# Kernel tuning notes

Measured on AMD Instinct MI355X. Metric: run time of the kernel, lower is better.

The kernel has to match this reference:

```python
import jax, jax.numpy as jnp
import numpy as np

NUM_HEADS = 8


def setup_inputs() -> dict:
    key = jax.random.key(0)
    k1, k2, k3 = jax.random.split(key, 3)
    B, C, H, W = 2, 256, 64, 64
    x = jax.random.normal(k1, (B, C, H, W), dtype=jnp.float32)
    # 1x1 conv kernels flattened to [out_ch, in_ch]
    w_qkv = jax.random.normal(k2, (3 * C, C), dtype=jnp.float32) * (1.0 / np.sqrt(C))
    w_proj = jax.random.normal(k3, (C, C), dtype=jnp.float32) * (1.0 / np.sqrt(C))
    return {"x": x, "w_qkv": w_qkv, "w_proj": w_proj}


def reference(x, w_qkv, w_proj):
    B, C, H, W = x.shape
    h = NUM_HEADS
    hc = C // h  # head_channels
    scale = hc ** (-0.5)

    # 1x1 conv == per-pixel matmul over channels
    qkv = jnp.einsum('bchw,oc->bohw', x, w_qkv)  # [B, 3C, H, W]
    q, k, v = jnp.split(qkv, 3, axis=1)          # each [B, C, H, W]

    def to_heads(t):
        # 'b (h c) x y -> b h (x y) c'
        return t.reshape(B, h, hc, H * W).transpose(0, 1, 3, 2)

    q, k, v = to_heads(q), to_heads(k), to_heads(v)  # [B, h, N, hc]

    attn = jax.nn.softmax(jnp.einsum('bhnc,bhmc->bhnm', q, k) * scale, axis=-1)
    out = jnp.einsum('bhnm,bhmc->bhnc', attn, v)     # [B, h, N, hc]

    # 'b h (x y) c -> b (h c) x y'
    out = out.transpose(0, 1, 3, 2).reshape(B, C, H, W)
    return jnp.einsum('bchw,oc->bohw', out, w_proj)
```

## Files before the change

### kernel.cpp

```cpp
#include <hip/hip_runtime.h>
#include <hip/hip_bf16.h>


typedef short s8v __attribute__((ext_vector_type(8)));
typedef float f32x16 __attribute__((ext_vector_type(16)));
typedef float f32x2 __attribute__((ext_vector_type(2)));
typedef unsigned int u32;
typedef unsigned int u32x4 __attribute__((ext_vector_type(4)));

__device__ __forceinline__ u32 cvt_pk_bf16(float lo, float hi){
  u32 d;
  asm("v_cvt_pk_bf16_f32 %0, %1, %2" : "=v"(d) : "v"(lo), "v"(hi));
  return d;
}

__device__ __forceinline__ int frag_off(int row, int c){
  return ((c>>4)<<9) + (((c>>3)&1)<<8) + (row<<3) + (c&7);
}

__global__ __launch_bounds__(256) void k_transpose_cast(const float* __restrict__ x,
                                                        __hip_bfloat16* __restrict__ xt){
  __shared__ float tile[64][65];
  const int b = blockIdx.z;
  const int c0 = blockIdx.y * 64, p0 = blockIdx.x * 64;
  const int tx = threadIdx.x & 63, ty = threadIdx.x >> 6;
  const float* src = x + ((size_t)b*256 + c0)*4096 + p0;
#pragma unroll
  for(int i=0;i<16;i++){
    int r = i*4 + ty;
    tile[r][tx] = src[(size_t)r*4096 + tx];
  }
  __syncthreads();
  __hip_bfloat16* dstb = xt + (size_t)b*1048576;
#pragma unroll
  for(int it=0; it<2; ++it){
    int id = it*256 + threadIdx.x;
    int pl = id & 63, cc = id >> 6;
    int c = c0 + cc*8;
    u32x4 wv;
    wv.x = cvt_pk_bf16(tile[cc*8+0][pl], tile[cc*8+1][pl]);
    wv.y = cvt_pk_bf16(tile[cc*8+2][pl], tile[cc*8+3][pl]);
    wv.z = cvt_pk_bf16(tile[cc*8+4][pl], tile[cc*8+5][pl]);
    wv.w = cvt_pk_bf16(tile[cc*8+6][pl], tile[cc*8+7][pl]);
    int panel = (p0 + pl) >> 5;
    *(u32x4*)(dstb + (size_t)panel*8192 + frag_off(pl & 31, c)) = wv;
  }
}

__global__ __launch_bounds__(256) void k_cast_w(const float* __restrict__ wqkv,
                                                const float* __restrict__ wproj,
                                                __hip_bfloat16* __restrict__ wq,
                                                __hip_bfloat16* __restrict__ wp){
  int e = blockIdx.x*256 + threadIdx.x;
  const float* srcw; __hip_bfloat16* dstw;
  if(e < 24576){ srcw = wqkv; dstw = wq; }
  else { e -= 24576; srcw = wproj; dstw = wp; }
  int o = e >> 5, c0 = (e & 31)*8;
  const float* s = srcw + (size_t)o*256 + c0;
  u32x4 wv;
  wv.x = cvt_pk_bf16(s[0], s[1]);
  wv.y = cvt_pk_bf16(s[2], s[3]);
  wv.z = cvt_pk_bf16(s[4], s[5]);
  wv.w = cvt_pk_bf16(s[6], s[7]);
  *(u32x4*)(dstw + (size_t)(o>>5)*8192 + frag_off(o & 31, c0)) = wv;
}

__global__ __launch_bounds__(256) void k_qkv(const __hip_bfloat16* __restrict__ w,
                                             const __hip_bfloat16* __restrict__ xt,
                                             __hip_bfloat16* __restrict__ qb,
                                             __hip_bfloat16* __restrict__ kb,
                                             __hip_bfloat16* __restrict__ vt){
  const int wave = threadIdx.x >> 6, lane = threadIdx.x & 63;
  const int l31 = lane & 31, hi = lane >> 5;
  const int t = blockIdx.x*4 + wave;
  const int ntp = t & 127, mtp = t >> 7;
  const __hip_bfloat16* a0 = w  + (size_t)(2*mtp)*8192 + lane*8;
  const __hip_bfloat16* b0 = xt + (size_t)(2*ntp)*8192 + lane*8;
  f32x16 acc00, acc01, acc10, acc11;
#pragma unroll
  for(int i=0;i<16;i++){ acc00[i]=0.f; acc01[i]=0.f; acc10[i]=0.f; acc11[i]=0.f; }
#pragma unroll
  for(int kk=0;kk<16;kk++){
    s8v af0 = *(const s8v*)(a0 + kk*512);
    s8v af1 = *(const s8v*)(a0 + 8192 + kk*512);
    s8v bf0 = *(const s8v*)(b0 + kk*512);
    s8v bf1 = *(const s8v*)(b0 + 8192 + kk*512);
    acc00 = __builtin_amdgcn_mfma_f32_32x32x16_bf16(af0, bf0, acc00, 0,0,0);
    acc01 = __builtin_amdgcn_mfma_f32_32x32x16_bf16(af0, bf1, acc01, 0,0,0);
    acc10 = __builtin_amdgcn_mfma_f32_32x32x16_bf16(af1, bf0, acc10, 0,0,0);
    acc11 = __builtin_amdgcn_mfma_f32_32x32x16_bf16(af1, bf1, acc11, 0,0,0);
  }
  const int region = mtp >> 2;
  const float s = (region==0) ? (0.17677669529663687f * 1.4426950408889634f) : 1.0f;
#pragma unroll
  for(int mi=0; mi<2; ++mi){
#pragma unroll
    for(int ni=0; ni<2; ++ni){
      const f32x16& acc = (mi==0) ? (ni==0?acc00:acc01) : (ni==0?acc10:acc11);
      const int mt = 2*mtp + mi, nt = 2*ntp + ni;
      const int bb = nt >> 7, ktile = nt & 127, h = mt & 7;
      const size_t tbase = (size_t)(bb*8 + h)*131072 + (size_t)ktile*1024;
      if(region < 2){
        __hip_bfloat16* dst = (region==0 ? qb : kb) + tbase + l31*8 + 4*hi;
#pragma unroll
        for(int g=0; g<4; ++g){
          uint2 wv;
          wv.x = cvt_pk_bf16(acc[4*g+0]*s, acc[4*g+1]*s);
          wv.y = cvt_pk_bf16(acc[4*g+2]*s, acc[4*g+3]*s);
          *(uint2*)(dst + (g>>1)*512 + (g&1)*256) = wv;
        }
      } else {
        const int j = l31 >> 4, hv = (l31 >> 2) & 1, tt = ((l31>>3)&1)*4 + (l31&3);
        __hip_bfloat16* dst = vt + tbase + j*512 + hv*256 + tt;
#pragma unroll
        for(int r=0;r<16;++r){
          int c = (r&3) + 8*(r>>2) + 4*hi;
          dst[c*8] = __float2bfloat16(acc[r]);
        }
      }
    }
  }
}

__global__ __launch_bounds__(256) void k_attn(const __hip_bfloat16* __restrict__ qb,
                                              const __hip_bfloat16* __restrict__ kb,
                                              const __hip_bfloat16* __restrict__ vt,
                                              __hip_bfloat16* __restrict__ ost){
  __shared__ float part[4][32][33];
  __shared__ float lsl[4][32];
  const int wave = threadIdx.x >> 6, lane = threadIdx.x & 63;
  const int l31 = lane & 31, hi = lane >> 5;
  const int bh = blockIdx.x >> 7, qc = blockIdx.x & 127;

  const __hip_bfloat16* qt = qb + (size_t)bh*131072 + (size_t)qc*1024 + (size_t)lane*8;
  const s8v qf0 = *(const s8v*)qt;
  const s8v qf1 = *(const s8v*)(qt + 512);

  const __hip_bfloat16* kbase = kb + (size_t)bh*131072 + (size_t)lane*8;
  const __hip_bfloat16* vbase = vt + (size_t)bh*131072 + (size_t)lane*8;

  f32x16 zf;
#pragma unroll
  for(int i=0;i<16;i++) zf[i]=0.f;
  f32x16 oacc;
#pragma unroll
  for(int i=0;i<16;i++) oacc[i]=0.f;
  f32x2 s0 = {0.f,0.f}, s1 = {0.f,0.f}, s2 = {0.f,0.f}, s3 = {0.f,0.f};

  const int kt0 = wave*32;
#pragma unroll 2
  for(int i=0;i<32;++i){
    const int kt = kt0 + i;
    const __hip_bfloat16* kp = kbase + (size_t)kt*1024;
    s8v kf0 = *(const s8v*)kp, kf1 = *(const s8v*)(kp + 512);
    f32x16 sa = __builtin_amdgcn_mfma_f32_32x32x16_bf16(kf0, qf0, zf, 0,0,0);
    sa = __builtin_amdgcn_mfma_f32_32x32x16_bf16(kf1, qf1, sa, 0,0,0);

    float pv[16];
#pragma unroll
    for(int r=0;r<16;++r) pv[r] = __builtin_amdgcn_exp2f(sa[r]);
    s0 += (f32x2){pv[0],pv[1]};  s1 += (f32x2){pv[2],pv[3]};
    s2 += (f32x2){pv[4],pv[5]};  s3 += (f32x2){pv[6],pv[7]};
    s0 += (f32x2){pv[8],pv[9]};  s1 += (f32x2){pv[10],pv[11]};
    s2 += (f32x2){pv[12],pv[13]}; s3 += (f32x2){pv[14],pv[15]};

    u32x4 w0, w1;
    w0.x = cvt_pk_bf16(pv[0],  pv[1]);   w0.y = cvt_pk_bf16(pv[2],  pv[3]);
    w0.z = cvt_pk_bf16(pv[4],  pv[5]);   w0.w = cvt_pk_bf16(pv[6],  pv[7]);
    w1.x = cvt_pk_bf16(pv[8],  pv[9]);   w1.y = cvt_pk_bf16(pv[10], pv[11]);
    w1.z = cvt_pk_bf16(pv[12], pv[13]);  w1.w = cvt_pk_bf16(pv[14], pv[15]);
    s8v pa0 = __builtin_bit_cast(s8v, w0);
    s8v pa1 = __builtin_bit_cast(s8v, w1);

    const __hip_bfloat16* vp = vbase + (size_t)kt*1024;
    s8v vf0 = *(const s8v*)vp, vf1 = *(const s8v*)(vp + 512);
    oacc = __builtin_amdgcn_mfma_f32_32x32x16_bf16(vf0, pa0, oacc, 0,0,0);
    oacc = __builtin_amdgcn_mfma_f32_32x32x16_bf16(vf1, pa1, oacc, 0,0,0);
  }

  float lsum = (s0.x + s0.y) + (s1.x + s1.y) + (s2.x + s2.y) + (s3.x + s3.y);
  lsum += __shfl_xor(lsum, 32, 64);
  lsl[wave][l31] = lsum;
#pragma unroll
  for(int r=0;r<16;++r){
    int c = (r&3) + 8*(r>>2) + 4*hi;
    part[wave][l31][c] = oacc[r];
  }
  __syncthreads();

  const int b = bh >> 3, h = bh & 7;
  __hip_bfloat16* obase = ost + (size_t)(b*128 + qc)*8192;
#pragma unroll
  for(int it=0; it<4; ++it){
    int e = it*256 + threadIdx.x;
    int q = e >> 5, c = e & 31;
    float o = (part[0][q][c] + part[1][q][c]) + (part[2][q][c] + part[3][q][c]);
    float L = (lsl[0][q] + lsl[1][q]) + (lsl[2][q] + lsl[3][q]);
    obase[(h*2 + (c>>4))*512 + ((c>>3)&1)*256 + q*8 + (c&7)] = __float2bfloat16(o / L);
  }
}

__global__ __launch_bounds__(256) void k_proj(const __hip_bfloat16* __restrict__ w,
                                              const __hip_bfloat16* __restrict__ ost,
                                              float* __restrict__ out){
  const int wave = threadIdx.x >> 6, lane = threadIdx.x & 63;
  const int l31 = lane & 31, hi = lane >> 5;
  const int t = blockIdx.x*4 + wave;
  const int nt = t & 255, mt = t >> 8;
  const __hip_bfloat16* arow = w   + (size_t)mt*8192 + lane*8;
  const __hip_bfloat16* brow = ost + (size_t)nt*8192 + lane*8;
  f32x16 acc;
#pragma unroll
  for(int i=0;i<16;i++) acc[i]=0.f;
#pragma unroll
  for(int kk=0;kk<16;kk++){
    s8v a = *(const s8v*)(arow + kk*512);
    s8v b = *(const s8v*)(brow + kk*512);
    acc = __builtin_amdgcn_mfma_f32_32x32x16_bf16(a, b, acc, 0,0,0);
  }
  const int pg = nt*32 + l31;
  const int bb = pg >> 12, p = pg & 4095;
  float* dst = out + (size_t)bb*1048576 + p;
#pragma unroll
  for(int r=0;r<16;++r){
    int o = mt*32 + (r&3) + 8*(r>>2) + 4*hi;
    dst[(size_t)o*4096] = acc[r];
  }
}

extern "C" void kernel_launch(void* const* d_in, const int* in_sizes, int n_in,
                              void* d_out, int out_size, void* d_ws, size_t ws_size,
                              hipStream_t stream){
  const float* x     = (const float*)d_in[0];
  const float* wqkv  = (const float*)d_in[1];
  const float* wproj = (const float*)d_in[2];
  float* out = (float*)d_out;

  const size_t SZ_XT = (size_t)8192*256*2;
  const size_t SZ_VT = (size_t)16*32*4096*2;
  const size_t SZ_WQ = (size_t)768*256*2;
  const size_t SZ_WP = (size_t)256*256*2;
  if(ws_size < SZ_XT + SZ_VT + SZ_WQ + SZ_WP) return;

  char* ws = (char*)d_ws;
  __hip_bfloat16* xt  = (__hip_bfloat16*)ws;
  __hip_bfloat16* vt  = (__hip_bfloat16*)(ws + SZ_XT);
  __hip_bfloat16* wqb = (__hip_bfloat16*)(ws + SZ_XT + SZ_VT);
  __hip_bfloat16* wpb = (__hip_bfloat16*)(ws + SZ_XT + SZ_VT + SZ_WQ);
  __hip_bfloat16* qb  = (__hip_bfloat16*)d_out;
  __hip_bfloat16* kb  = qb + (size_t)2*1024*1024;
  __hip_bfloat16* ost = xt;

  k_cast_w<<<128, 256, 0, stream>>>(wqkv, wproj, wqb, wpb);
  k_transpose_cast<<<dim3(64,4,2), 256, 0, stream>>>(x, xt);
  k_qkv<<<384, 256, 0, stream>>>(wqb, xt, qb, kb, vt);
  k_attn<<<2048, 256, 0, stream>>>(qb, kb, vt, ost);
  k_proj<<<512, 256, 0, stream>>>(wpb, ost, out);
}
```

Measured before the change: 85.28 us.

## Process two query tiles per attention block to reuse K/V fragments

Each attention block now handles 64 queries (two 32-query tiles) instead of 32. Each loaded K and V fragment feeds two sets of MFMAs, which halves K/V global traffic per query and halves the grid. Block indices are also remapped so that consecutive blocks spread across batch-heads, which may help L2/XCD locality. The cost is doubled accumulator and score register pressure, with launch bounds set to 4 blocks per CU, and fewer blocks in flight.

```diff
diff --git a/kernel.cpp b/kernel.cpp
--- a/kernel.cpp
+++ b/kernel.cpp
@@ -122,19 +122,22 @@
   }
 }
 
-__global__ __launch_bounds__(256) void k_attn(const __hip_bfloat16* __restrict__ qb,
-                                              const __hip_bfloat16* __restrict__ kb,
-                                              const __hip_bfloat16* __restrict__ vt,
-                                              __hip_bfloat16* __restrict__ ost){
-  __shared__ float part[4][32][33];
-  __shared__ float lsl[4][32];
+__global__ __launch_bounds__(256, 4) void k_attn(const __hip_bfloat16* __restrict__ qb,
+                                                 const __hip_bfloat16* __restrict__ kb,
+                                                 const __hip_bfloat16* __restrict__ vt,
+                                                 __hip_bfloat16* __restrict__ ost){
+  __shared__ float part[4][64][33];
+  __shared__ float lsl[4][64];
   const int wave = threadIdx.x >> 6, lane = threadIdx.x & 63;
   const int l31 = lane & 31, hi = lane >> 5;
-  const int bh = blockIdx.x >> 7, qc = blockIdx.x & 127;
-
-  const __hip_bfloat16* qt = qb + (size_t)bh*131072 + (size_t)qc*1024 + (size_t)lane*8;
-  const s8v qf0 = *(const s8v*)qt;
-  const s8v qf1 = *(const s8v*)(qt + 512);
+  const int vid = (blockIdx.x & 7)*128 + (blockIdx.x >> 3);
+  const int bh = vid >> 6, qc = vid & 63;
+
+  const __hip_bfloat16* qt = qb + (size_t)bh*131072 + (size_t)(qc*2)*1024 + (size_t)lane*8;
+  const s8v qfA0 = *(const s8v*)qt;
+  const s8v qfA1 = *(const s8v*)(qt + 512);
+  const s8v qfB0 = *(const s8v*)(qt + 1024);
+  const s8v qfB1 = *(const s8v*)(qt + 1536);
 
   const __hip_bfloat16* kbase = kb + (size_t)bh*131072 + (size_t)lane*8;
   const __hip_bfloat16* vbase = vt + (size_t)bh*131072 + (size_t)lane*8;
@@ -142,10 +145,10 @@
   f32x16 zf;
 #pragma unroll
   for(int i=0;i<16;i++) zf[i]=0.f;
-  f32x16 oacc;
-#pragma unroll
-  for(int i=0;i<16;i++) oacc[i]=0.f;
-  f32x2 s0 = {0.f,0.f}, s1 = {0.f,0.f}, s2 = {0.f,0.f}, s3 = {0.f,0.f};
+  f32x16 oaccA, oaccB;
+#pragma unroll
+  for(int i=0;i<16;i++){ oaccA[i]=0.f; oaccB[i]=0.f; }
+  f32x2 sA0={0.f,0.f}, sA1={0.f,0.f}, sB0={0.f,0.f}, sB1={0.f,0.f};
 
   const int kt0 = wave*32;
 #pragma unroll 2
@@ -153,50 +156,67 @@
     const int kt = kt0 + i;
     const __hip_bfloat16* kp = kbase + (size_t)kt*1024;
     s8v kf0 = *(const s8v*)kp, kf1 = *(const s8v*)(kp + 512);
-    f32x16 sa = __builtin_amdgcn_mfma_f32_32x32x16_bf16(kf0, qf0, zf, 0,0,0);
-    sa = __builtin_amdgcn_mfma_f32_32x32x16_bf16(kf1, qf1, sa, 0,0,0);
-
-    float pv[16];
-#pragma unroll
-    for(int r=0;r<16;++r) pv[r] = __builtin_amdgcn_exp2f(sa[r]);
-    s0 += (f32x2){pv[0],pv[1]};  s1 += (f32x2){pv[2],pv[3]};
-    s2 += (f32x2){pv[4],pv[5]};  s3 += (f32x2){pv[6],pv[7]};
-    s0 += (f32x2){pv[8],pv[9]};  s1 += (f32x2){pv[10],pv[11]};
-    s2 += (f32x2){pv[12],pv[13]}; s3 += (f32x2){pv[14],pv[15]};
-
-    u32x4 w0, w1;
-    w0.x = cvt_pk_bf16(pv[0],  pv[1]);   w0.y = cvt_pk_bf16(pv[2],  pv[3]);
-    w0.z = cvt_pk_bf16(pv[4],  pv[5]);   w0.w = cvt_pk_bf16(pv[6],  pv[7]);
-    w1.x = cvt_pk_bf16(pv[8],  pv[9]);   w1.y = cvt_pk_bf16(pv[10], pv[11]);
-    w1.z = cvt_pk_bf16(pv[12], pv[13]);  w1.w = cvt_pk_bf16(pv[14], pv[15]);
-    s8v pa0 = __builtin_bit_cast(s8v, w0);
-    s8v pa1 = __builtin_bit_cast(s8v, w1);
+    f32x16 saA = __builtin_amdgcn_mfma_f32_32x32x16_bf16(kf0, qfA0, zf, 0,0,0);
+    saA = __builtin_amdgcn_mfma_f32_32x32x16_bf16(kf1, qfA1, saA, 0,0,0);
+    f32x16 saB = __builtin_amdgcn_mfma_f32_32x32x16_bf16(kf0, qfB0, zf, 0,0,0);
+    saB = __builtin_amdgcn_mfma_f32_32x32x16_bf16(kf1, qfB1, saB, 0,0,0);
+
+    float pvA[16], pvB[16];
+#pragma unroll
+    for(int r=0;r<16;++r) pvA[r] = __builtin_amdgcn_exp2f(saA[r]);
+#pragma unroll
+    for(int r=0;r<16;++r) pvB[r] = __builtin_amdgcn_exp2f(saB[r]);
+    sA0 += (f32x2){pvA[0],pvA[1]};   sA1 += (f32x2){pvA[2],pvA[3]};
+    sA0 += (f32x2){pvA[4],pvA[5]};   sA1 += (f32x2){pvA[6],pvA[7]};
+    sA0 += (f32x2){pvA[8],pvA[9]};   sA1 += (f32x2){pvA[10],pvA[11]};
+    sA0 += (f32x2){pvA[12],pvA[13]}; sA1 += (f32x2){pvA[14],pvA[15]};
+    sB0 += (f32x2){pvB[0],pvB[1]};   sB1 += (f32x2){pvB[2],pvB[3]};
+    sB0 += (f32x2){pvB[4],pvB[5]};   sB1 += (f32x2){pvB[6],pvB[7]};
+    sB0 += (f32x2){pvB[8],pvB[9]};   sB1 += (f32x2){pvB[10],pvB[11]};
+    sB0 += (f32x2){pvB[12],pvB[13]}; sB1 += (f32x2){pvB[14],pvB[15]};
+
+    u32x4 wA0, wA1, wB0, wB1;
+    wA0.x = cvt_pk_bf16(pvA[0],  pvA[1]);   wA0.y = cvt_pk_bf16(pvA[2],  pvA[3]);
+    wA0.z = cvt_pk_bf16(pvA[4],  pvA[5]);   wA0.w = cvt_pk_bf16(pvA[6],  pvA[7]);
+    wA1.x = cvt_pk_bf16(pvA[8],  pvA[9]);   wA1.y = cvt_pk_bf16(pvA[10], pvA[11]);
+    wA1.z = cvt_pk_bf16(pvA[12], pvA[13]);  wA1.w = cvt_pk_bf16(pvA[14], pvA[15]);
+    wB0.x = cvt_pk_bf16(pvB[0],  pvB[1]);   wB0.y = cvt_pk_bf16(pvB[2],  pvB[3]);
+    wB0.z = cvt_pk_bf16(pvB[4],  pvB[5]);   wB0.w = cvt_pk_bf16(pvB[6],  pvB[7]);
+    wB1.x = cvt_pk_bf16(pvB[8],  pvB[9]);   wB1.y = cvt_pk_bf16(pvB[10], pvB[11]);
+    wB1.z = cvt_pk_bf16(pvB[12], pvB[13]);  wB1.w = cvt_pk_bf16(pvB[14], pvB[15]);
 
     const __hip_bfloat16* vp = vbase + (size_t)kt*1024;
     s8v vf0 = *(const s8v*)vp, vf1 = *(const s8v*)(vp + 512);
-    oacc = __builtin_amdgcn_mfma_f32_32x32x16_bf16(vf0, pa0, oacc, 0,0,0);
-    oacc = __builtin_amdgcn_mfma_f32_32x32x16_bf16(vf1, pa1, oacc, 0,0,0);
-  }
-
-  float lsum = (s0.x + s0.y) + (s1.x + s1.y) + (s2.x + s2.y) + (s3.x + s3.y);
-  lsum += __shfl_xor(lsum, 32, 64);
-  lsl[wave][l31] = lsum;
+    oaccA = __builtin_amdgcn_mfma_f32_32x32x16_bf16(vf0, __builtin_bit_cast(s8v, wA0), oaccA, 0,0,0);
+    oaccA = __builtin_amdgcn_mfma_f32_32x32x16_bf16(vf1, __builtin_bit_cast(s8v, wA1), oaccA, 0,0,0);
+    oaccB = __builtin_amdgcn_mfma_f32_32x32x16_bf16(vf0, __builtin_bit_cast(s8v, wB0), oaccB, 0,0,0);
+    oaccB = __builtin_amdgcn_mfma_f32_32x32x16_bf16(vf1, __builtin_bit_cast(s8v, wB1), oaccB, 0,0,0);
+  }
+
+  float lsumA = (sA0.x + sA0.y) + (sA1.x + sA1.y);
+  float lsumB = (sB0.x + sB0.y) + (sB1.x + sB1.y);
+  lsumA += __shfl_xor(lsumA, 32, 64);
+  lsumB += __shfl_xor(lsumB, 32, 64);
+  lsl[wave][l31] = lsumA;
+  lsl[wave][32 + l31] = lsumB;
 #pragma unroll
   for(int r=0;r<16;++r){
     int c = (r&3) + 8*(r>>2) + 4*hi;
-    part[wave][l31][c] = oacc[r];
+    part[wave][l31][c] = oaccA[r];
+    part[wave][32 + l31][c] = oaccB[r];
   }
   __syncthreads();
 
   const int b = bh >> 3, h = bh & 7;
-  __hip_bfloat16* obase = ost + (size_t)(b*128 + qc)*8192;
-#pragma unroll
-  for(int it=0; it<4; ++it){
+  __hip_bfloat16* obase = ost + (size_t)(b*128 + qc*2)*8192;
+#pragma unroll
+  for(int it=0; it<8; ++it){
     int e = it*256 + threadIdx.x;
     int q = e >> 5, c = e & 31;
     float o = (part[0][q][c] + part[1][q][c]) + (part[2][q][c] + part[3][q][c]);
     float L = (lsl[0][q] + lsl[1][q]) + (lsl[2][q] + lsl[3][q]);
-    obase[(h*2 + (c>>4))*512 + ((c>>3)&1)*256 + q*8 + (c&7)] = __float2bfloat16(o / L);
+    obase[(size_t)(q>>5)*8192 + (h*2 + (c>>4))*512 + ((c>>3)&1)*256 + (q&31)*8 + (c&7)]
+        = __float2bfloat16(o / L);
   }
 }
 
@@ -254,6 +274,6 @@
   k_cast_w<<<128, 256, 0, stream>>>(wqkv, wproj, wqb, wpb);
   k_transpose_cast<<<dim3(64,4,2), 256, 0, stream>>>(x, xt);
   k_qkv<<<384, 256, 0, stream>>>(wqb, xt, qb, kb, vt);
-  k_attn<<<2048, 256, 0, stream>>>(qb, kb, vt, ost);
+  k_attn<<<1024, 256, 0, stream>>>(qb, kb, vt, ost);
   k_proj<<<512, 256, 0, stream>>>(wpb, ost, out);
 }
```

Result: faster. 76.39 us (-10.4%).
